# Kernel tuning notes

Measured on AMD Instinct MI355X. Metric: run time of the kernel, lower is better.

The kernel has to match this reference:

```python
import jax, jax.numpy as jnp
import numpy as np

D_MODEL = 768
NUM_HEADS = 12
NUM_REG = 4
EPS = 1e-5


def _layernorm(x, g, b):
    mu = jnp.mean(x, axis=-1, keepdims=True)
    var = jnp.mean(jnp.square(x - mu), axis=-1, keepdims=True)
    return (x - mu) * jax.lax.rsqrt(var + EPS) * g + b


def _make_mask(seq_len):
    # True = masked (disallowed), matching torch attn_mask bool semantics.
    r1 = 1 + NUM_REG
    mask = np.ones((seq_len, seq_len), dtype=bool)
    mask[0, :] = False                      # context token attends to all
    mask[1:r1, :] = False                   # register tokens attend to all
    mask[r1:, :r1] = False                  # (not use_input_context_token) == False
    mask[r1:, r1:] = ~np.eye(seq_len - r1, dtype=bool)  # feature tokens: self only
    return jnp.asarray(mask)


def setup_inputs() -> dict:
    key = jax.random.key(0)
    ks = jax.random.split(key, 16)
    B, C, H, W = 8, D_MODEL, 32, 32
    d = D_MODEL
    s = 0.02
    inp = {
        "x": jax.random.normal(ks[0], (B, C, H, W), jnp.float32),
        "context_token": jax.random.normal(ks[1], (B, 1, d), jnp.float32),
        "register_tokens": jax.random.normal(ks[2], (B, NUM_REG, d), jnp.float32),
        "in_proj_w": jax.random.normal(ks[3], (3 * d, d), jnp.float32) * s,
        "in_proj_b": jnp.zeros((3 * d,), jnp.float32),
        "out_w": jax.random.normal(ks[4], (d, d), jnp.float32) * s,
        "out_b": jnp.zeros((d,), jnp.float32),
        "ln1_g": jnp.ones((d,), jnp.float32),
        "ln1_b": jnp.zeros((d,), jnp.float32),
        "ln2_g": jnp.ones((d,), jnp.float32),
        "ln2_b": jnp.zeros((d,), jnp.float32),
        "w1": jax.random.normal(ks[5], (4 * d, d), jnp.float32) * s,
        "b1": jnp.zeros((4 * d,), jnp.float32),
        "w2": jax.random.normal(ks[6], (d, 4 * d), jnp.float32) * s,
        "b2": jnp.zeros((d,), jnp.float32),
    }
    return inp


def reference(x, context_token, register_tokens, in_proj_w, in_proj_b,
              out_w, out_b, ln1_g, ln1_b, ln2_g, ln2_b, w1, b1, w2, b2):
    B, C, H, W = x.shape
    d, nh = D_MODEL, NUM_HEADS
    hd = d // nh
    x_flat = x.reshape(B, C, H * W).transpose(0, 2, 1)          # [B, HW, d]
    tokens = jnp.concatenate([context_token, register_tokens], axis=1)
    xw = _layernorm(jnp.concatenate([tokens, x_flat], axis=1), ln1_g, ln1_b)  # [B, S, d]
    S = xw.shape[1]

    qkv = xw @ in_proj_w.T + in_proj_b                           # [B, S, 3d]
    q, k, v = jnp.split(qkv, 3, axis=-1)
    q = q.reshape(B, S, nh, hd).transpose(0, 2, 1, 3)            # [B, nh, S, hd]
    k = k.reshape(B, S, nh, hd).transpose(0, 2, 1, 3)
    v = v.reshape(B, S, nh, hd).transpose(0, 2, 1, 3)

    scores = jnp.einsum("bhqd,bhkd->bhqk", q, k) / jnp.sqrt(jnp.float32(hd))
    mask = _make_mask(S)
    scores = jnp.where(mask, jnp.float32(-1e9), scores)
    probs = jax.nn.softmax(scores, axis=-1)
    attn = jnp.einsum("bhqk,bhkd->bhqd", probs, v)               # [B, nh, S, hd]
    attn = attn.transpose(0, 2, 1, 3).reshape(B, S, d)
    attn = attn @ out_w.T + out_b

    h1 = attn + xw                                                # residual
    ff = _layernorm(h1, ln2_g, ln2_b)
    ff = jax.nn.gelu(ff @ w1.T + b1, approximate=False) @ w2.T + b2
    out = ff + h1                                                 # [B, S, d]

    r1 = 1 + NUM_REG
    ctx_out = out[:, 0:1, :]
    reg_out = out[:, 1:r1, :]
    feat_out = out[:, r1:, :].transpose(0, 2, 1).reshape(B, C, H, W)
    return feat_out, ctx_out, reg_out
```

## Files before the change

kernel.cpp:

```cpp
#include <hip/hip_runtime.h>
#include <math.h>
#include <stdint.h>

#define SEQ 1029
#define BATCH 8
#define M_TOT (BATCH * SEQ)
#define M_PAD 8320
#define NCHUNK 17

typedef float floatx4 __attribute__((ext_vector_type(4)));
typedef __bf16 bf16x8 __attribute__((ext_vector_type(8)));

__device__ __forceinline__ unsigned short f2bf(float f) {
  union { float f; unsigned u; } v; v.f = f;
  unsigned r = v.u + 0x7fffu + ((v.u >> 16) & 1u);
  return (unsigned short)(r >> 16);
}
__device__ __forceinline__ float bf2f(unsigned short h) {
  union { unsigned u; float f; } v; v.u = ((unsigned)h) << 16;
  return v.f;
}
__device__ __forceinline__ float bf_lo(unsigned u) { union { unsigned x; float f; } v; v.x = u << 16; return v.f; }
__device__ __forceinline__ float bf_hi(unsigned u) { union { unsigned x; float f; } v; v.x = u & 0xffff0000u; return v.f; }

__device__ __forceinline__ float wave_sum(float v) {
#pragma unroll
  for (int off = 32; off > 0; off >>= 1) v += __shfl_xor(v, off, 64);
  return v;
}
__device__ __forceinline__ float wave_max(float v) {
#pragma unroll
  for (int off = 32; off > 0; off >>= 1) v = fmaxf(v, __shfl_xor(v, off, 64));
  return v;
}

__device__ __forceinline__ float fast_gelu(float v) {
  const float ax = fabsf(v) * 0.70710678118654752f;
  const float t = __builtin_amdgcn_rcpf(1.0f + 0.3275911f * ax);
  const float poly = ((((1.061405429f * t - 1.453152027f) * t + 1.421413741f) * t
                       - 0.284496736f) * t + 0.254829592f) * t;
  const float er = 1.0f - poly * __expf(-ax * ax);
  return 0.5f * v * (1.0f + copysignf(er, v));
}

__device__ __forceinline__ void gload16(const unsigned short* g, unsigned short* l) {
  __builtin_amdgcn_global_load_lds(
      (const __attribute__((address_space(1))) unsigned int*)g,
      (__attribute__((address_space(3))) unsigned int*)l, 16, 0, 0);
}

template <int C>
__device__ __forceinline__ void vwait() {
  if constexpr (C == 0) asm volatile("s_waitcnt vmcnt(0)" ::: "memory");
  else if constexpr (C == 4) asm volatile("s_waitcnt vmcnt(4)" ::: "memory");
  else asm volatile("s_waitcnt vmcnt(8)" ::: "memory");
}

#define NQ_QKV 442368
#define NQ_OUT 147456
#define NQ_W1  589824
#define NQ_W2  589824
#define NQ_PAD 8448
__global__ void convert_all(const float4* __restrict__ inw, const float4* __restrict__ outw,
                            const float4* __restrict__ w1, const float4* __restrict__ w2,
                            ushort4* __restrict__ wqkv, ushort4* __restrict__ wout,
                            ushort4* __restrict__ w1b, ushort4* __restrict__ w2b,
                            ushort4* __restrict__ xw_pad, ushort4* __restrict__ attn_pad) {
  const int i = blockIdx.x * 256 + threadIdx.x;
  const float4* src; ushort4* dst; int off;
  if (i < NQ_QKV) { src = inw; dst = wqkv; off = i; }
  else if (i < NQ_QKV + NQ_OUT) { src = outw; dst = wout; off = i - NQ_QKV; }
  else if (i < NQ_QKV + NQ_OUT + NQ_W1) { src = w1; dst = w1b; off = i - NQ_QKV - NQ_OUT; }
  else if (i < NQ_QKV + NQ_OUT + NQ_W1 + NQ_W2) { src = w2; dst = w2b; off = i - NQ_QKV - NQ_OUT - NQ_W1; }
  else {
    const int j = i - (NQ_QKV + NQ_OUT + NQ_W1 + NQ_W2);
    const ushort4 z = {0, 0, 0, 0};
    if (j < NQ_PAD) { xw_pad[j] = z; attn_pad[j] = z; }
    return;
  }
  const float4 v = src[off];
  ushort4 o;
  o.x = f2bf(v.x); o.y = f2bf(v.y); o.z = f2bf(v.z); o.w = f2bf(v.w);
  dst[off] = o;
}
#define NQ_ALL (NQ_QKV + NQ_OUT + NQ_W1 + NQ_W2 + NQ_PAD)

__global__ __launch_bounds__(256) void ln1_feat(const float* __restrict__ x,
                                                const float* __restrict__ g,
                                                const float* __restrict__ bta,
                                                unsigned short* __restrict__ xw) {
  __shared__ float tile[768 * 17];
  const int b = blockIdx.y;
  const int hw0 = blockIdx.x * 16;
  const int t = threadIdx.x;
  const float* xb = x + (size_t)b * 768 * 1024;
  const int cl = t >> 4, hl = t & 15;
  for (int it = 0; it < 48; it++) {
    const int c = it * 16 + cl;
    tile[c * 17 + hl] = xb[(size_t)c * 1024 + hw0 + hl];
  }
  __syncthreads();
  const int wave = t >> 6, lane = t & 63;
  for (int tk = wave; tk < 16; tk += 4) {
    float vals[12], s = 0.f, ss = 0.f;
#pragma unroll
    for (int i = 0; i < 12; i++) {
      const float v = tile[(lane + 64 * i) * 17 + tk];
      vals[i] = v; s += v; ss += v * v;
    }
    s = wave_sum(s); ss = wave_sum(ss);
    const float mu = s * (1.0f / 768.0f);
    const float var = ss * (1.0f / 768.0f) - mu * mu;
    const float rs = rsqrtf(var + 1e-5f);
    const int row = b * SEQ + 5 + hw0 + tk;
    unsigned short* orow = xw + (size_t)row * 768;
#pragma unroll
    for (int i = 0; i < 12; i++) {
      const int c = lane + 64 * i;
      orow[c] = f2bf((vals[i] - mu) * rs * g[c] + bta[c]);
    }
  }
}

__global__ __launch_bounds__(256) void ln1_special(const float* __restrict__ ctx,
                                                   const float* __restrict__ regs,
                                                   const float* __restrict__ g,
                                                   const float* __restrict__ bta,
                                                   unsigned short* __restrict__ xw) {
  const int gw = blockIdx.x * 4 + (threadIdx.x >> 6);
  const int lane = threadIdx.x & 63;
  if (gw >= 40) return;
  const int b = gw / 5, s = gw % 5;
  const float* src = (s == 0) ? (ctx + (size_t)b * 768)
                              : (regs + ((size_t)b * 4 + (s - 1)) * 768);
  float vals[12], sm = 0.f, ss = 0.f;
#pragma unroll
  for (int i = 0; i < 12; i++) {
    const float v = src[lane + 64 * i];
    vals[i] = v; sm += v; ss += v * v;
  }
  sm = wave_sum(sm); ss = wave_sum(ss);
  const float mu = sm * (1.0f / 768.0f);
  const float var = ss * (1.0f / 768.0f) - mu * mu;
  const float rs = rsqrtf(var + 1e-5f);
  unsigned short* orow = xw + (size_t)(b * SEQ + s) * 768;
#pragma unroll
  for (int i = 0; i < 12; i++) {
    const int c = lane + 64 * i;
    orow[c] = f2bf((vals[i] - mu) * rs * g[c] + bta[c]);
  }
}

#define BM 128
#define BN 128
#define BK 32

template <int EPI, int K, int N, int NBUF>
__global__ __launch_bounds__(256, NBUF == 3 ? 3 : 2) void gemm_bt(
    const unsigned short* __restrict__ A,
    const unsigned short* __restrict__ W,
    const float* __restrict__ bias,
    const unsigned short* __restrict__ residb,
    const float* __restrict__ residf,
    float* __restrict__ outf,
    unsigned short* __restrict__ outb) {
  __shared__ alignas(16) unsigned short As[NBUF][BM * BK];
  __shared__ alignas(16) unsigned short Ws[NBUF][BN * BK];
  const int t = threadIdx.x;
  const int wave = t >> 6, lane = t & 63;
  const int quad = lane >> 4, l16 = lane & 15;
  const int wm = (wave & 1) * 64, wn = (wave >> 1) * 64;

  constexpr int GX = N / BN;
  constexpr int NWG = GX * (M_PAD / BM);
  constexpr int Q8 = NWG / 8, R8 = NWG % 8;
  const int flat = blockIdx.y * GX + blockIdx.x;
  const int xcd = flat & 7, idx = flat >> 3;
  const int wgid = (xcd < R8 ? xcd * (Q8 + 1) : R8 * (Q8 + 1) + (xcd - R8) * Q8) + idx;
  const int tileM = (wgid / GX) * BM;
  const int tileN = (wgid % GX) * BN;

  const int rl = lane >> 2;
  const int kc8 = ((lane & 3) ^ ((rl >> 1) & 3)) * 8;
  const unsigned short* Ag = A + (size_t)(tileM + wave * 16 + rl) * K;
  const unsigned short* Wg = W + (size_t)(tileN + wave * 16 + rl) * K;
  const int ldst = wave * 512 + lane * 8;

  const int koff = ((quad ^ ((l16 >> 1) & 3)) * 8);

  const floatx4 zero4 = {0.f, 0.f, 0.f, 0.f};
  floatx4 acc[4][4];
#pragma unroll
  for (int i = 0; i < 4; i++)
#pragma unroll
    for (int j = 0; j < 4; j++) acc[i][j] = zero4;

  auto dma = [&](int k0, int buf) {
    gload16(Ag + k0 + kc8, &As[buf][0] + ldst);
    gload16(Ag + (size_t)64 * K + k0 + kc8, &As[buf][0] + ldst + 2048);
    gload16(Wg + k0 + kc8, &Ws[buf][0] + ldst);
    gload16(Wg + (size_t)64 * K + k0 + kc8, &Ws[buf][0] + ldst + 2048);
  };
  auto compute = [&](int buf) {
    bf16x8 af[4], wf[4];
#pragma unroll
    for (int i = 0; i < 4; i++)
      af[i] = *(const bf16x8*)(&As[buf][0] + (wm + i * 16 + l16) * BK + koff);
#pragma unroll
    for (int j = 0; j < 4; j++)
      wf[j] = *(const bf16x8*)(&Ws[buf][0] + (wn + j * 16 + l16) * BK + koff);
#pragma unroll
    for (int i = 0; i < 4; i++)
#pragma unroll
      for (int j = 0; j < 4; j++)
        acc[i][j] = __builtin_amdgcn_mfma_f32_16x16x32_bf16(af[i], wf[j], acc[i][j], 0, 0, 0);
  };

  constexpr int NSTEP = K / BK;
  constexpr int PF = NBUF - 1;

#pragma unroll
  for (int p = 0; p < PF; ++p) dma(p * BK, p);

  int cb = 0, db = PF % NBUF;
#pragma unroll 1
  for (int i = 0; i < NSTEP - PF; ++i) {
    vwait<4 * (NBUF - 2)>();
    __builtin_amdgcn_s_barrier();
    __builtin_amdgcn_sched_barrier(0);
    dma((i + PF) * BK, db);
    db = (db + 1 == NBUF) ? 0 : db + 1;
    compute(cb);
    cb = (cb + 1 == NBUF) ? 0 : cb + 1;
  }
  if constexpr (NBUF == 4) {
    vwait<8>(); __builtin_amdgcn_s_barrier(); __builtin_amdgcn_sched_barrier(0);
    compute(cb); cb = (cb + 1 == NBUF) ? 0 : cb + 1;
  }
  vwait<4>(); __builtin_amdgcn_s_barrier(); __builtin_amdgcn_sched_barrier(0);
  compute(cb); cb = (cb + 1 == NBUF) ? 0 : cb + 1;
  vwait<0>(); __builtin_amdgcn_s_barrier(); __builtin_amdgcn_sched_barrier(0);
  compute(cb);

#pragma unroll
  for (int i = 0; i < 4; i++) {
    const int mbase = tileM + wm + i * 16 + quad * 4;
#pragma unroll
    for (int j = 0; j < 4; j++) {
      const int n = tileN + wn + j * 16 + l16;
      const float bv = bias[n];
#pragma unroll
      for (int r = 0; r < 4; r++) {
        const size_t idx2 = (size_t)(mbase + r) * N + n;
        float v = acc[i][j][r] + bv;
        if constexpr (EPI == 0) {
          outb[idx2] = f2bf(v);
        } else if constexpr (EPI == 1) {
          outf[idx2] = v + bf2f(residb[idx2]);
        } else if constexpr (EPI == 2) {
          outb[idx2] = f2bf(fast_gelu(v));
        } else {
          outf[idx2] = v + residf[idx2];
        }
      }
    }
  }
}

#define BM2 256
#define BN2 256

template <int EPI, int K, int N>
__global__ __launch_bounds__(512, 2) void gemm_big(
    const unsigned short* __restrict__ A,
    const unsigned short* __restrict__ W,
    const float* __restrict__ bias,
    unsigned short* __restrict__ outb) {
  __shared__ alignas(16) unsigned short As[4][BM2 * BK];
  __shared__ alignas(16) unsigned short Ws[4][BN2 * BK];
  const int t = threadIdx.x;
  const int wave = t >> 6, lane = t & 63;
  const int quad = lane >> 4, l16 = lane & 15;
  const int wm = (wave & 1) * 128, wn = (wave >> 1) * 64;

  constexpr int GX = N / BN2;
  constexpr int GY = (M_PAD + BM2 - 1) / BM2;
  constexpr int NWG = GX * GY;
  constexpr int Q8 = NWG / 8, R8 = NWG % 8;
  const int flat = blockIdx.y * GX + blockIdx.x;
  const int xcd = flat & 7, idx = flat >> 3;
  const int wgid = (xcd < R8 ? xcd * (Q8 + 1) : R8 * (Q8 + 1) + (xcd - R8) * Q8) + idx;
  const int tileM = (wgid / GX) * BM2;
  const int tileN = (wgid % GX) * BN2;

  const int rl = lane >> 2;
  const int kc8 = ((lane & 3) ^ ((rl >> 1) & 3)) * 8;
  const unsigned short* Ag = A + (size_t)(tileM + wave * 16 + rl) * K;
  const unsigned short* Wg = W + (size_t)(tileN + wave * 16 + rl) * K;
  const int ldst = wave * 512 + lane * 8;

  const int koff = ((quad ^ ((l16 >> 1) & 3)) * 8);

  const floatx4 zero4 = {0.f, 0.f, 0.f, 0.f};
  floatx4 acc[8][4];
#pragma unroll
  for (int i = 0; i < 8; i++)
#pragma unroll
    for (int j = 0; j < 4; j++) acc[i][j] = zero4;

  auto dma = [&](int k0, int buf) {
    gload16(Ag + k0 + kc8, &As[buf][0] + ldst);
    gload16(Ag + (size_t)128 * K + k0 + kc8, &As[buf][0] + ldst + 4096);
    gload16(Wg + k0 + kc8, &Ws[buf][0] + ldst);
    gload16(Wg + (size_t)128 * K + k0 + kc8, &Ws[buf][0] + ldst + 4096);
  };
  auto compute = [&](int buf) {
    bf16x8 af[8], wf[4];
#pragma unroll
    for (int i = 0; i < 8; i++)
      af[i] = *(const bf16x8*)(&As[buf][0] + (wm + i * 16 + l16) * BK + koff);
#pragma unroll
    for (int j = 0; j < 4; j++)
      wf[j] = *(const bf16x8*)(&Ws[buf][0] + (wn + j * 16 + l16) * BK + koff);
#pragma unroll
    for (int i = 0; i < 8; i++)
#pragma unroll
      for (int j = 0; j < 4; j++)
        acc[i][j] = __builtin_amdgcn_mfma_f32_16x16x32_bf16(af[i], wf[j], acc[i][j], 0, 0, 0);
  };

  constexpr int NSTEP = K / BK;
  constexpr int PF = 3;

  dma(0, 0); dma(BK, 1); dma(2 * BK, 2);

  int cb = 0, db = 3;
#pragma unroll 1
  for (int i = 0; i < NSTEP - PF; ++i) {
    vwait<8>();
    __builtin_amdgcn_s_barrier();
    __builtin_amdgcn_sched_barrier(0);
    dma((i + PF) * BK, db);
    db = (db + 1) & 3;
    compute(cb);
    cb = (cb + 1) & 3;
  }
  vwait<8>(); __builtin_amdgcn_s_barrier(); __builtin_amdgcn_sched_barrier(0);
  compute(cb); cb = (cb + 1) & 3;
  vwait<4>(); __builtin_amdgcn_s_barrier(); __builtin_amdgcn_sched_barrier(0);
  compute(cb); cb = (cb + 1) & 3;
  vwait<0>(); __builtin_amdgcn_s_barrier(); __builtin_amdgcn_sched_barrier(0);
  compute(cb);

#pragma unroll
  for (int i = 0; i < 8; i++) {
    const int mbase = tileM + wm + i * 16 + quad * 4;
#pragma unroll
    for (int j = 0; j < 4; j++) {
      const int n = tileN + wn + j * 16 + l16;
      const float bv = bias[n];
#pragma unroll
      for (int r = 0; r < 4; r++) {
        if (mbase + r < M_PAD) {
          const size_t idx2 = (size_t)(mbase + r) * N + n;
          float v = acc[i][j][r] + bv;
          if constexpr (EPI == 2) v = fast_gelu(v);
          outb[idx2] = f2bf(v);
        }
      }
    }
  }
}

__global__ __launch_bounds__(256) void attn_feat(const unsigned short* __restrict__ qkv,
                                                 unsigned short* __restrict__ attn) {
  __shared__ float kk[5][64];
  __shared__ float vv[5][64];
  const int b = blockIdx.z, h = blockIdx.y;
  const int t = threadIdx.x;
  const size_t base = (size_t)b * SEQ;
  for (int i = t; i < 320; i += 256) {
    const int j = i >> 6, dd = i & 63;
    const size_t rb = (base + j) * 2304 + (size_t)h * 64 + dd;
    kk[j][dd] = bf2f(qkv[rb + 768]);
    vv[j][dd] = bf2f(qkv[rb + 1536]);
  }
  __syncthreads();
  const int wave = t >> 6, lane = t & 63;
  const int s = 5 + blockIdx.x * 4 + wave;
  const size_t row = (base + s) * 2304 + (size_t)h * 64;
  const float q = bf2f(qkv[row + lane]);
  const float kself = bf2f(qkv[row + 768 + lane]);
  const float vself = bf2f(qkv[row + 1536 + lane]);
  float sc[6];
#pragma unroll
  for (int j = 0; j < 5; j++) sc[j] = wave_sum(q * kk[j][lane]) * 0.125f;
  sc[5] = wave_sum(q * kself) * 0.125f;
  float mx = sc[0];
#pragma unroll
  for (int j = 1; j < 6; j++) mx = fmaxf(mx, sc[j]);
  float den = 0.f, e[6];
#pragma unroll
  for (int j = 0; j < 6; j++) { e[j] = expf(sc[j] - mx); den += e[j]; }
  const float inv = 1.0f / den;
  float o = 0.f;
#pragma unroll
  for (int j = 0; j < 5; j++) o += e[j] * vv[j][lane];
  o += e[5] * vself;
  attn[(base + s) * 768 + (size_t)h * 64 + lane] = f2bf(o * inv);
}

__global__ __launch_bounds__(256) void attn_part(const unsigned short* __restrict__ qkv,
                                                 float* __restrict__ part) {
  __shared__ float qs[5][64];
  __shared__ float sc[5][64];
  __shared__ float mArr[5], lArr[5];
  __shared__ float og[4][320];
  const int c = blockIdx.x, h = blockIdx.y, b = blockIdx.z;
  const int t = threadIdx.x;
  const size_t base = (size_t)b * SEQ;
  const int kbase = (c < 16) ? (5 + 64 * c) : 0;
  const int nvalid = (c < 16) ? 64 : 5;

  for (int i = t; i < 320; i += 256)
    qs[i >> 6][i & 63] = bf2f(qkv[(base + (i >> 6)) * 2304 + (size_t)h * 64 + (i & 63)]);
  __syncthreads();

  const int keyloc = t >> 2, dc = t & 3;
  const int key = kbase + keyloc;
  const unsigned short* krow = qkv + (base + key) * 2304 + 768 + (size_t)h * 64;
  const uint4 k0 = *(const uint4*)(krow + dc * 8);
  const uint4 k1 = *(const uint4*)(krow + dc * 8 + 32);
  float kf[16];
  {
    const unsigned ku[8] = {k0.x, k0.y, k0.z, k0.w, k1.x, k1.y, k1.z, k1.w};
#pragma unroll
    for (int j = 0; j < 8; j++) { kf[2 * j] = bf_lo(ku[j]); kf[2 * j + 1] = bf_hi(ku[j]); }
  }
#pragma unroll
  for (int q = 0; q < 5; q++) {
    const float* qp = qs[q];
    float d0 = 0.f;
#pragma unroll
    for (int j = 0; j < 8; j++) d0 += qp[dc * 8 + j] * kf[j];
#pragma unroll
    for (int j = 0; j < 8; j++) d0 += qp[dc * 8 + 32 + j] * kf[8 + j];
    d0 += __shfl_xor(d0, 1, 64);
    d0 += __shfl_xor(d0, 2, 64);
    if (dc == 0) sc[q][keyloc] = (keyloc < nvalid) ? d0 * 0.125f : -1e30f;
  }
  __syncthreads();

  const int wave = t >> 6, lane = t & 63;
  for (int q = wave; q < 5; q += 4) {
    const float v = sc[q][lane];
    const float m = wave_max(v);
    const float e = expf(v - m);
    sc[q][lane] = e;
    const float l = wave_sum(e);
    if (lane == 0) { mArr[q] = m; lArr[q] = l; }
  }
  __syncthreads();

  const int d = t & 63, g = t >> 6;
  float o[5] = {0.f, 0.f, 0.f, 0.f, 0.f};
  for (int i = 0; i < 16; i++) {
    const int kl = g * 16 + i;
    const float v = bf2f(qkv[(base + kbase + kl) * 2304 + 1536 + (size_t)h * 64 + d]);
#pragma unroll
    for (int q = 0; q < 5; q++) o[q] += sc[q][kl] * v;
  }
#pragma unroll
  for (int q = 0; q < 5; q++) og[g][q * 64 + d] = o[q];
  __syncthreads();

  float* pw = part + (size_t)((b * 12 + h) * NCHUNK + c) * 5 * 66;
  for (int i = t; i < 320; i += 256) {
    const int q = i >> 6, dd = i & 63;
    pw[q * 66 + 2 + dd] = og[0][i] + og[1][i] + og[2][i] + og[3][i];
    if (dd == 0) { pw[q * 66] = mArr[q]; pw[q * 66 + 1] = lArr[q]; }
  }
}

__global__ __launch_bounds__(64) void attn_comb(const float* __restrict__ part,
                                                unsigned short* __restrict__ attn) {
  const int qi = blockIdx.x, h = blockIdx.y, b = blockIdx.z;
  const int d = threadIdx.x;
  float M = -3e38f, L = 0.f, o = 0.f;
  for (int c = 0; c < NCHUNK; c++) {
    const float* p = part + ((size_t)((b * 12 + h) * NCHUNK + c) * 5 + qi) * 66;
    const float mc = p[0], lc = p[1], oc = p[2 + d];
    if (mc > M) {
      const float s = expf(M - mc);
      L = L * s + lc; o = o * s + oc; M = mc;
    } else {
      const float w = expf(mc - M);
      L += lc * w; o += oc * w;
    }
  }
  attn[((size_t)b * SEQ + qi) * 768 + (size_t)h * 64 + d] = f2bf(o / L);
}

__global__ __launch_bounds__(256) void ln2_kernel(const float* __restrict__ h1,
                                                  const float* __restrict__ g,
                                                  const float* __restrict__ bta,
                                                  unsigned short* __restrict__ out) {
  const int row = blockIdx.x * 4 + (threadIdx.x >> 6);
  const int lane = threadIdx.x & 63;
  const float* r = h1 + (size_t)row * 768;
  float vals[12], sm = 0.f, ss = 0.f;
#pragma unroll
  for (int i = 0; i < 12; i++) {
    const float v = r[lane + 64 * i];
    vals[i] = v; sm += v; ss += v * v;
  }
  sm = wave_sum(sm); ss = wave_sum(ss);
  const float mu = sm * (1.0f / 768.0f);
  const float var = ss * (1.0f / 768.0f) - mu * mu;
  const float rs = rsqrtf(var + 1e-5f);
  unsigned short* orow = out + (size_t)row * 768;
#pragma unroll
  for (int i = 0; i < 12; i++) {
    const int c = lane + 64 * i;
    orow[c] = f2bf((vals[i] - mu) * rs * g[c] + bta[c]);
  }
}

__global__ __launch_bounds__(256) void scatter_all(const float* __restrict__ outb,
                                                   float* __restrict__ dout) {
  const int t = threadIdx.x;
  const int b = blockIdx.z;
  if (blockIdx.x == 24) {
    const int i = (b * 32 + blockIdx.y) * 256 + t;
    if (i >= 40 * 768) return;
    const int rowi = i / 768, c = i % 768;
    const int bb = rowi / 5, s = rowi % 5;
    const float v = outb[(size_t)(bb * SEQ + s) * 768 + c];
    if (s == 0) dout[6291456 + (size_t)bb * 768 + c] = v;
    else dout[6291456 + 6144 + ((size_t)bb * 4 + (s - 1)) * 768 + c] = v;
    return;
  }
  __shared__ float tl[32][33];
  const int hw0 = blockIdx.y * 32, c0 = blockIdx.x * 32;
  const int i = t >> 5, j = t & 31;
#pragma unroll
  for (int r = 0; r < 4; r++) {
    const int hwi = i + r * 8;
    tl[hwi][j] = outb[(size_t)(b * SEQ + 5 + hw0 + hwi) * 768 + c0 + j];
  }
  __syncthreads();
#pragma unroll
  for (int r = 0; r < 4; r++) {
    const int ci = i + r * 8;
    dout[(size_t)b * 768 * 1024 + (size_t)(c0 + ci) * 1024 + hw0 + j] = tl[j][ci];
  }
}

extern "C" void kernel_launch(void* const* d_in, const int* in_sizes, int n_in,
                              void* d_out, int out_size, void* d_ws, size_t ws_size,
                              hipStream_t stream) {
  const float* x    = (const float*)d_in[0];
  const float* ctx  = (const float*)d_in[1];
  const float* regs = (const float*)d_in[2];
  const float* inw  = (const float*)d_in[3];
  const float* inb  = (const float*)d_in[4];
  const float* outw = (const float*)d_in[5];
  const float* outbi= (const float*)d_in[6];
  const float* ln1g = (const float*)d_in[7];
  const float* ln1b = (const float*)d_in[8];
  const float* ln2g = (const float*)d_in[9];
  const float* ln2b = (const float*)d_in[10];
  const float* w1   = (const float*)d_in[11];
  const float* b1   = (const float*)d_in[12];
  const float* w2   = (const float*)d_in[13];
  const float* b2   = (const float*)d_in[14];

  char* ws = (char*)d_ws;
  unsigned short* wqkv_b = (unsigned short*)(ws + 0);
  unsigned short* wout_b = (unsigned short*)(ws + 3538944);
  unsigned short* w1_b   = (unsigned short*)(ws + 4718592);
  unsigned short* w2_b   = (unsigned short*)(ws + 9437184);
  unsigned short* xw_b   = (unsigned short*)(ws + 14155776);
  unsigned short* ln2o_b = (unsigned short*)(ws + 26935296);
  float*          h1_f   = (float*)(ws + 39714816);
  unsigned short* qkv_b  = (unsigned short*)(ws + 65273856);
  unsigned short* attn_b = (unsigned short*)(ws + 103612416);
  float*          out_f  = (float*)(ws + 14155776);
  unsigned short* ffm_b  = (unsigned short*)(ws + 65273856);
  float*          part_f = (float*)(ws + 39714816);
  float* dout = (float*)d_out;

  convert_all<<<(NQ_ALL + 255) / 256, 256, 0, stream>>>(
      (const float4*)inw, (const float4*)outw, (const float4*)w1, (const float4*)w2,
      (ushort4*)wqkv_b, (ushort4*)wout_b, (ushort4*)w1_b, (ushort4*)w2_b,
      (ushort4*)(xw_b + (size_t)M_TOT * 768), (ushort4*)(attn_b + (size_t)M_TOT * 768));

  ln1_feat<<<dim3(64, 8), 256, 0, stream>>>(x, ln1g, ln1b, xw_b);
  ln1_special<<<10, 256, 0, stream>>>(ctx, regs, ln1g, ln1b, xw_b);

  gemm_bt<0, 768, 2304, 3><<<dim3(2304 / BN, M_PAD / BM), 256, 0, stream>>>(
      xw_b, wqkv_b, inb, nullptr, nullptr, nullptr, qkv_b);

  attn_feat<<<dim3(256, 12, 8), 256, 0, stream>>>(qkv_b, attn_b);
  attn_part<<<dim3(NCHUNK, 12, 8), 256, 0, stream>>>(qkv_b, part_f);
  attn_comb<<<dim3(5, 12, 8), 64, 0, stream>>>(part_f, attn_b);

  gemm_bt<1, 768, 768, 4><<<dim3(768 / BN, M_PAD / BM), 256, 0, stream>>>(
      attn_b, wout_b, outbi, xw_b, nullptr, h1_f, nullptr);

  ln2_kernel<<<M_PAD / 4, 256, 0, stream>>>(h1_f, ln2g, ln2b, ln2o_b);

  gemm_big<2, 768, 3072><<<dim3(3072 / BN2, (M_PAD + BM2 - 1) / BM2), 512, 0, stream>>>(
      ln2o_b, w1_b, b1, ffm_b);

  gemm_bt<3, 3072, 768, 4><<<dim3(768 / BN, M_PAD / BM), 256, 0, stream>>>(
      ffm_b, w2_b, b2, nullptr, h1_f, out_f, nullptr);

  scatter_all<<<dim3(25, 32, 8), 256, 0, stream>>>(out_f, dout);
}
```

Measured before the change: 435.9 us.

## Restructure FFN1 GEMM into double-buffered 64-wide K tiles with half-step pipelining

The big FFN1 GEMM moves from a 4-deep ring of 32-wide K buffers with prefetch distance 3 to a 2-deep double buffer of 64-wide K tiles. Each tile is split into two 32-wide halves, and a barrier sits between the halves. MFMA blocks are wrapped in s_setprio to favour the math waves, and A fragments are loaded in two groups of four to lower register pressure. The aim is finer interleaving of loads and MFMAs with fewer live fragments, at the cost of a shallower prefetch and more barriers per K step. The last iteration issues a redundant wrap-around prefetch of tile 0, which is harmless but wasted traffic.

```diff
diff --git a/kernel.cpp b/kernel.cpp
--- a/kernel.cpp
+++ b/kernel.cpp
@@ -271,13 +271,13 @@
 #define BN2 256
 
 template <int EPI, int K, int N>
-__global__ __launch_bounds__(512, 2) void gemm_big(
+__global__ __launch_bounds__(512, 2) void gemm_8p(
     const unsigned short* __restrict__ A,
     const unsigned short* __restrict__ W,
     const float* __restrict__ bias,
     unsigned short* __restrict__ outb) {
-  __shared__ alignas(16) unsigned short As[4][BM2 * BK];
-  __shared__ alignas(16) unsigned short Ws[4][BN2 * BK];
+  __shared__ alignas(16) unsigned short As[2][2][256 * 32];
+  __shared__ alignas(16) unsigned short Ws[2][2][256 * 32];
   const int t = threadIdx.x;
   const int wave = t >> 6, lane = t & 63;
   const int quad = lane >> 4, l16 = lane & 15;
@@ -295,9 +295,9 @@
 
   const int rl = lane >> 2;
   const int kc8 = ((lane & 3) ^ ((rl >> 1) & 3)) * 8;
-  const unsigned short* Ag = A + (size_t)(tileM + wave * 16 + rl) * K;
-  const unsigned short* Wg = W + (size_t)(tileN + wave * 16 + rl) * K;
-  const int ldst = wave * 512 + lane * 8;
+  const unsigned short* Ag = A + (size_t)(tileM + wave * 32 + rl) * K;
+  const unsigned short* Wg = W + (size_t)(tileN + wave * 32 + rl) * K;
+  const int ldst = wave * 1024 + lane * 8;
 
   const int koff = ((quad ^ ((l16 >> 1) & 3)) * 8);
 
@@ -308,53 +308,68 @@
 #pragma unroll
     for (int j = 0; j < 4; j++) acc[i][j] = zero4;
 
-  auto dma = [&](int k0, int buf) {
-    gload16(Ag + k0 + kc8, &As[buf][0] + ldst);
-    gload16(Ag + (size_t)128 * K + k0 + kc8, &As[buf][0] + ldst + 4096);
-    gload16(Wg + k0 + kc8, &Ws[buf][0] + ldst);
-    gload16(Wg + (size_t)128 * K + k0 + kc8, &Ws[buf][0] + ldst + 4096);
+  auto stage = [&](int tt, int kh, int buf) {
+    const int k0 = tt * 64 + kh * 32;
+    const unsigned short* a = Ag + k0 + kc8;
+    const unsigned short* w = Wg + k0 + kc8;
+    unsigned short* la = &As[buf][kh][0] + ldst;
+    unsigned short* lw = &Ws[buf][kh][0] + ldst;
+    gload16(a, la);
+    gload16(a + (size_t)16 * K, la + 512);
+    gload16(w, lw);
+    gload16(w + (size_t)16 * K, lw + 512);
   };
-  auto compute = [&](int buf) {
-    bf16x8 af[8], wf[4];
-#pragma unroll
-    for (int i = 0; i < 8; i++)
-      af[i] = *(const bf16x8*)(&As[buf][0] + (wm + i * 16 + l16) * BK + koff);
+  auto computeG = [&](int buf, int kh) {
+    const unsigned short* Ab = &As[buf][kh][0];
+    const unsigned short* Wb = &Ws[buf][kh][0];
+    bf16x8 wf[4], af[4];
 #pragma unroll
     for (int j = 0; j < 4; j++)
-      wf[j] = *(const bf16x8*)(&Ws[buf][0] + (wn + j * 16 + l16) * BK + koff);
-#pragma unroll
-    for (int i = 0; i < 8; i++)
-#pragma unroll
-      for (int j = 0; j < 4; j++)
-        acc[i][j] = __builtin_amdgcn_mfma_f32_16x16x32_bf16(af[i], wf[j], acc[i][j], 0, 0, 0);
+      wf[j] = *(const bf16x8*)(Wb + (wn + j * 16 + l16) * 32 + koff);
+#pragma unroll
+    for (int ih = 0; ih < 2; ih++) {
+#pragma unroll
+      for (int i = 0; i < 4; i++)
+        af[i] = *(const bf16x8*)(Ab + (wm + ih * 64 + i * 16 + l16) * 32 + koff);
+      __builtin_amdgcn_s_setprio(1);
+#pragma unroll
+      for (int i = 0; i < 4; i++)
+#pragma unroll
+        for (int j = 0; j < 4; j++)
+          acc[ih * 4 + i][j] =
+              __builtin_amdgcn_mfma_f32_16x16x32_bf16(af[i], wf[j], acc[ih * 4 + i][j], 0, 0, 0);
+      __builtin_amdgcn_s_setprio(0);
+    }
   };
 
-  constexpr int NSTEP = K / BK;
-  constexpr int PF = 3;
-
-  dma(0, 0); dma(BK, 1); dma(2 * BK, 2);
-
-  int cb = 0, db = 3;
+  constexpr int NT = K / 64;
+
+  stage(0, 0, 0);
+  stage(0, 1, 0);
+
+  int cur = 0;
 #pragma unroll 1
-  for (int i = 0; i < NSTEP - PF; ++i) {
-    vwait<8>();
+  for (int tt = 0; tt < NT; ++tt) {
+    const int nx = (tt + 1 < NT) ? tt + 1 : 0;
+    const int nb = cur ^ 1;
+    vwait<4>();
     __builtin_amdgcn_s_barrier();
     __builtin_amdgcn_sched_barrier(0);
-    dma((i + PF) * BK, db);
-    db = (db + 1) & 3;
-    compute(cb);
-    cb = (cb + 1) & 3;
-  }
-  vwait<8>(); __builtin_amdgcn_s_barrier(); __builtin_amdgcn_sched_barrier(0);
-  compute(cb); cb = (cb + 1) & 3;
-  vwait<4>(); __builtin_amdgcn_s_barrier(); __builtin_amdgcn_sched_barrier(0);
-  compute(cb); cb = (cb + 1) & 3;
-  vwait<0>(); __builtin_amdgcn_s_barrier(); __builtin_amdgcn_sched_barrier(0);
-  compute(cb);
-
-#pragma unroll
-  for (int i = 0; i < 8; i++) {
-    const int mbase = tileM + wm + i * 16 + quad * 4;
+    stage(nx, 0, nb);
+    computeG(cur, 0);
+    vwait<4>();
+    __builtin_amdgcn_s_barrier();
+    __builtin_amdgcn_sched_barrier(0);
+    stage(nx, 1, nb);
+    computeG(cur, 1);
+    cur = nb;
+  }
+  vwait<0>();
+  __builtin_amdgcn_s_barrier();
+
+#pragma unroll
+  for (int a = 0; a < 8; a++) {
+    const int mbase = tileM + wm + (a >> 2) * 64 + (a & 3) * 16 + quad * 4;
 #pragma unroll
     for (int j = 0; j < 4; j++) {
       const int n = tileN + wn + j * 16 + l16;
@@ -363,7 +378,7 @@
       for (int r = 0; r < 4; r++) {
         if (mbase + r < M_PAD) {
           const size_t idx2 = (size_t)(mbase + r) * N + n;
-          float v = acc[i][j][r] + bv;
+          float v = acc[a][j][r] + bv;
           if constexpr (EPI == 2) v = fast_gelu(v);
           outb[idx2] = f2bf(v);
         }
@@ -610,7 +625,7 @@
 
   ln2_kernel<<<M_PAD / 4, 256, 0, stream>>>(h1_f, ln2g, ln2b, ln2o_b);
 
-  gemm_big<2, 768, 3072><<<dim3(3072 / BN2, (M_PAD + BM2 - 1) / BM2), 512, 0, stream>>>(
+  gemm_8p<2, 768, 3072><<<dim3(3072 / BN2, (M_PAD + BM2 - 1) / BM2), 512, 0, stream>>>(
       ln2o_b, w1_b, b1, ffm_b);
 
   gemm_bt<3, 3072, 768, 4><<<dim3(768 / BN, M_PAD / BM), 256, 0, stream>>>(
```

Result: no change. 430.0 us (-1.4%).
